# Kernel optimization log

Hardware: AMD Instinct MI355X
Metric: run time of the kernel (lower is better)

The kernel has to match this reference:

```python
import jax, jax.numpy as jnp
import numpy as np

B, S, D, H = 8, 384, 768, 12
MAX_POS = 512
P = 2 * MAX_POS - 1  # 1023


def setup_inputs() -> dict:
    key = jax.random.key(0)
    ks = jax.random.split(key, 14)
    w = 0.02
    return {
        "x": jax.random.normal(ks[0], (B, S, D), jnp.float32),
        "rel_pos_emb": jax.random.normal(ks[1], (P, D), jnp.float32),
        "Wq": jax.random.normal(ks[2], (D, D), jnp.float32) * w,
        "bq": jax.random.normal(ks[3], (D,), jnp.float32) * w,
        "Wk": jax.random.normal(ks[4], (D, D), jnp.float32) * w,
        "bk": jax.random.normal(ks[5], (D,), jnp.float32) * w,
        "Wv": jax.random.normal(ks[6], (D, D), jnp.float32) * w,
        "bv": jax.random.normal(ks[7], (D,), jnp.float32) * w,
        "q_bias": jax.random.normal(ks[8], (D,), jnp.float32) * w,
        "v_bias": jax.random.normal(ks[9], (D,), jnp.float32) * w,
        "Wpk": jax.random.normal(ks[10], (D, D), jnp.float32) * w,
        "Wpq": jax.random.normal(ks[11], (D, D), jnp.float32) * w,
        "Wo": jax.random.normal(ks[12], (D, D), jnp.float32) * w,
        "bo": jax.random.normal(ks[13], (D,), jnp.float32) * w,
    }


def reference(x, rel_pos_emb, Wq, bq, Wk, bk, Wv, bv, q_bias, v_bias, Wpk, Wpq, Wo, bo):
    b, s, d = x.shape
    dh = d // H
    scale = dh ** -0.5
    # relative position index: rel[i, j] = j - i + MAX_POS - 1
    rel = (jnp.arange(s)[None, :] - jnp.arange(s)[:, None]) + MAX_POS - 1
    emb = rel_pos_emb[rel]                      # [S, S, D]
    q = (x @ Wq + bq + q_bias).reshape(b, s, H, dh)
    k = (x @ Wk + bk).reshape(b, s, H, dh)
    v = (x @ Wv + bv + v_bias).reshape(b, s, H, dh)
    Kp = (emb @ Wpk).reshape(s, s, H, dh)       # pos keys   [i, j, h, d]
    Qp = (emb @ Wpq).reshape(s, s, H, dh)       # pos queries[i, j, h, d]
    c2c = jnp.einsum('bihd,bjhd->bhij', q, k)
    c2p = jnp.einsum('bihd,ijhd->bhij', q, Kp)
    p2c = jnp.einsum('ijhd,bjhd->bhij', Qp, k)
    scores = (c2c + c2p + p2c) * scale          # [B, H, S, S]
    w = jax.nn.softmax(scores, axis=-1)
    out = jnp.einsum('bhij,bjhd->bihd', w, v).reshape(b, s, d)
    return out @ Wo + bo
```

## Files before the change

kernel.cpp:

```cpp
#include <hip/hip_runtime.h>
#include <hip/hip_bf16.h>
#include <math.h>

#define BATCH 8
#define SEQ 384
#define DIM 768
#define NH 12
#define DH 64
#define NPOS 767
#define POS_OFF 128
#define NTOK (BATCH * SEQ)
#define QKN 1536
#define QKVN 2304
#define PN 1536

typedef __attribute__((ext_vector_type(8))) short short8;
typedef __attribute__((ext_vector_type(4))) float floatx4;
typedef unsigned int u32;

__device__ __forceinline__ ushort f2bf(float f) {
    __hip_bfloat16 h = __float2bfloat16(f);
    return *reinterpret_cast<ushort*>(&h);
}

__device__ __forceinline__ void gld16(const ushort* g, ushort* l) {
    __builtin_amdgcn_global_load_lds(
        (const __attribute__((address_space(1))) u32*)g,
        (__attribute__((address_space(3))) u32*)l, 16, 0, 0);
}

__global__ void cvt_all(const float* __restrict__ x, const float* __restrict__ rpe,
                        ushort* __restrict__ xb, ushort* __restrict__ rpeb) {
    int idx = blockIdx.x * 256 + threadIdx.x;
    const int n4x = NTOK * DIM / 4;
    const int n4p = NPOS * DIM / 4;
    const float* src; ushort* dst; int j;
    if (idx < n4x) { src = x; dst = xb; j = idx; }
    else if (idx < n4x + n4p) { src = rpe + (size_t)POS_OFF * DIM; dst = rpeb; j = idx - n4x; }
    else return;
    float4 f = ((const float4*)src)[j];
    ushort o[4] = {f2bf(f.x), f2bf(f.y), f2bf(f.z), f2bf(f.w)};
    *(uint2*)&dst[(size_t)j * 4] = *(uint2*)o;
}

__global__ __launch_bounds__(256) void cvt_transpose6(
    const float* W0, const float* W1, const float* W2,
    const float* W3, const float* W4, const float* W5,
    ushort* __restrict__ dst)
{
    __shared__ float t[64][65];
    const float* srcs[6] = {W0, W1, W2, W3, W4, W5};
    const float* in = srcs[blockIdx.z];
    ushort* out = dst + (size_t)blockIdx.z * DIM * DIM;
    const int tid = threadIdx.x;
    const int r0 = blockIdx.y * 64, c0 = blockIdx.x * 64;
    for (int p = 0; p < 16; ++p) {
        int e = tid + p * 256, i = e >> 6, j = e & 63;
        t[i][j] = in[(size_t)(r0 + i) * DIM + c0 + j];
    }
    __syncthreads();
    for (int p = 0; p < 16; ++p) {
        int e = tid + p * 256, i = e >> 6, j = e & 63;
        out[(size_t)(c0 + i) * DIM + r0 + j] = f2bf(t[j][i]);
    }
}

__global__ __launch_bounds__(256) void gemm128_qkv(
    const ushort* __restrict__ A, const ushort* __restrict__ Bt,
    const float* __restrict__ bq, const float* __restrict__ qbias,
    const float* __restrict__ bk, const float* __restrict__ bv,
    const float* __restrict__ vbias,
    ushort* __restrict__ qk, ushort* __restrict__ vT)
{
    __shared__ ushort As[128 * 64];
    __shared__ ushort Bs[128 * 64];
    const int tid = threadIdx.x;
    const int lane = tid & 63, w = tid >> 6;
    const int n0 = blockIdx.x * 128, m0 = blockIdx.y * 128;
    const int lr = lane >> 3;
    const int lc = (lane & 7) ^ (lr & 7);
    const ushort* ga[4]; const ushort* gb[4];
#pragma unroll
    for (int p = 0; p < 4; ++p) {
        int row = (w * 4 + p) * 8 + lr;
        ga[p] = A + (size_t)(m0 + row) * DIM + lc * 8;
        gb[p] = Bt + (size_t)(n0 + row) * DIM + lc * 8;
    }
    floatx4 acc[4][4] = {};
    const int qr = (w >> 1) * 64, qc = (w & 1) * 64;
    const int lm = lane & 15, lk = lane >> 4;
    for (int k0 = 0; k0 < DIM; k0 += 64) {
#pragma unroll
        for (int p = 0; p < 4; ++p) {
            gld16(ga[p], As + (w * 4 + p) * 512);
            gld16(gb[p], Bs + (w * 4 + p) * 512);
            ga[p] += 64; gb[p] += 64;
        }
        __syncthreads();
#pragma unroll
        for (int kk = 0; kk < 2; ++kk) {
            int ch = (kk * 4 + lk) ^ (lm & 7);
            short8 af[4], bf[4];
#pragma unroll
            for (int t = 0; t < 4; ++t) {
                af[t] = *(const short8*)&As[(qr + t * 16 + lm) * 64 + ch * 8];
                bf[t] = *(const short8*)&Bs[(qc + t * 16 + lm) * 64 + ch * 8];
            }
#pragma unroll
            for (int i = 0; i < 4; ++i)
#pragma unroll
                for (int j = 0; j < 4; ++j)
                    acc[i][j] = __builtin_amdgcn_mfma_f32_16x16x32_bf16(af[i], bf[j], acc[i][j], 0, 0, 0);
        }
        __syncthreads();
    }
#pragma unroll
    for (int i = 0; i < 4; ++i) {
        int mbase = m0 + qr + i * 16 + (lane >> 4) * 4;
        int bb = mbase / SEQ;
        int s0 = mbase - bb * SEQ;
#pragma unroll
        for (int j = 0; j < 4; ++j) {
            int n = n0 + qc + j * 16 + lm;
            float bs;
            if (n < 768) bs = bq[n] + qbias[n];
            else if (n < QKN) bs = bk[n - 768];
            else bs = bv[n - QKN] + vbias[n - QKN];
            if (n < QKN) {
#pragma unroll
                for (int r = 0; r < 4; ++r)
                    qk[(size_t)(mbase + r) * QKN + n] = f2bf(acc[i][j][r] + bs);
            } else {
                int c = n - QKN, h = c >> 6, d = c & 63;
                ushort tmp[4];
#pragma unroll
                for (int r = 0; r < 4; ++r) tmp[r] = f2bf(acc[i][j][r] + bs);
                *(uint2*)&vT[(((size_t)bb * NH + h) * DH + d) * SEQ + s0] = *(uint2*)tmp;
            }
        }
    }
}

__global__ __launch_bounds__(256) void gemm_bf16(
    const ushort* __restrict__ A, const ushort* __restrict__ Bt,
    const float* __restrict__ b1,
    float* __restrict__ outF, ushort* __restrict__ outB,
    int M, int N, int K)
{
    __shared__ ushort As[64][72];
    __shared__ ushort Bs[64][72];
    const int tid = threadIdx.x;
    const int lane = tid & 63, wave = tid >> 6;
    const int m0 = blockIdx.y * 64, n0 = blockIdx.x * 64;
    floatx4 acc[4] = {};
    for (int k0 = 0; k0 < K; k0 += 64) {
        for (int p = 0; p < 2; ++p) {
            int e = tid + p * 256;
            int m = e >> 3, k8 = e & 7;
            uint4 val = {0, 0, 0, 0};
            if (m0 + m < M) val = *(const uint4*)(A + (size_t)(m0 + m) * K + k0 + k8 * 8);
            *(uint4*)&As[m][k8 * 8] = val;
            *(uint4*)&Bs[m][k8 * 8] = *(const uint4*)(Bt + (size_t)(n0 + m) * K + k0 + k8 * 8);
        }
        __syncthreads();
#pragma unroll
        for (int kk = 0; kk < 64; kk += 32) {
            short8 a = *(const short8*)&As[wave * 16 + (lane & 15)][kk + (lane >> 4) * 8];
#pragma unroll
            for (int c = 0; c < 4; ++c) {
                short8 b = *(const short8*)&Bs[c * 16 + (lane & 15)][kk + (lane >> 4) * 8];
                acc[c] = __builtin_amdgcn_mfma_f32_16x16x32_bf16(a, b, acc[c], 0, 0, 0);
            }
        }
        __syncthreads();
    }
#pragma unroll
    for (int c = 0; c < 4; ++c) {
        int col = n0 + c * 16 + (lane & 15);
        float bias = b1 ? b1[col] : 0.f;
#pragma unroll
        for (int r = 0; r < 4; ++r) {
            int row = m0 + wave * 16 + (lane >> 4) * 4 + r;
            if (row >= M) continue;
            float v = acc[c][r] + bias;
            if (outF) outF[(size_t)row * N + col] = v;
            if (outB) outB[(size_t)row * N + col] = f2bf(v);
        }
    }
}

__global__ __launch_bounds__(512, 4) void attn_fused2(
    const ushort* __restrict__ qk, const ushort* __restrict__ vT,
    const ushort* __restrict__ posKQ, ushort* __restrict__ aob)
{
    __shared__ ushort qs[64 * 64];
    __shared__ ushort kt[64 * 64];
    __shared__ ushort kps[128 * 64];
    __shared__ ushort qps[128 * 64];
    __shared__ ushort vtt[64 * 64];
    __shared__ alignas(16) char smem_st[64 * 66 * 4];
    __shared__ float rowsum[64];
    float* st = (float*)smem_st;
    ushort* pt = (ushort*)smem_st;

    const int tid = threadIdx.x;
    const int lane = tid & 63, w = tid >> 6;
    const int i0 = blockIdx.x * 64;
    const int h = blockIdx.y, b = blockIdx.z;
    const int lm = lane & 15, lq = lane >> 4;
    const int lr = lane >> 3, l8 = lane & 7;
    const int lc = l8 ^ (lr & 7);

    if (tid < 64) rowsum[tid] = 0.f;

    gld16(qk + (size_t)(b * SEQ + i0 + 8 * w + lr) * QKN + h * DH + lc * 8, qs + w * 512);
    const ushort* kb = qk + 768 + h * DH;
    const ushort* vb = vT + ((size_t)b * NH + h) * DH * SEQ;

    floatx4 occ[2] = {};
    const int exr = tid >> 3, exseg = tid & 7;

    for (int jt = 0; jt < 6; ++jt) {
        const int j0 = jt * 64;
        const int t0 = j0 - i0 + 320;
        gld16(kb + (size_t)(b * SEQ + j0 + 8 * w + lr) * QKN + lc * 8, kt + w * 512);
        gld16(posKQ + (size_t)(t0 + 16 * w + lr) * PN + h * DH + lc * 8, kps + w * 1024);
        gld16(posKQ + (size_t)(t0 + 16 * w + 8 + lr) * PN + h * DH + lc * 8, kps + w * 1024 + 512);
        gld16(posKQ + (size_t)(t0 + 16 * w + lr) * PN + 768 + h * DH + lc * 8, qps + w * 1024);
        gld16(posKQ + (size_t)(t0 + 16 * w + 8 + lr) * PN + 768 + h * DH + lc * 8, qps + w * 1024 + 512);
        gld16(vb + (size_t)(8 * w + lr) * SEQ + j0 + lc * 8, vtt + w * 512);
        __syncthreads();

#pragma unroll
        for (int s = 0; s < 2; ++s) {
            int idx = w * 2 + s, tr = idx >> 2, tc = idx & 3;
            floatx4 a = {};
#pragma unroll
            for (int kk = 0; kk < 2; ++kk) {
                int ch = (kk * 4 + lq) ^ (lm & 7);
                short8 av = *(const short8*)&qs[(tr * 16 + lm) * 64 + ch * 8];
                short8 bv = *(const short8*)&kt[(tc * 16 + lm) * 64 + ch * 8];
                a = __builtin_amdgcn_mfma_f32_16x16x32_bf16(av, bv, a, 0, 0, 0);
            }
            int col = tc * 16 + lm;
#pragma unroll
            for (int r = 0; r < 4; ++r)
                st[(tr * 16 + lq * 4 + r) * 66 + col] = a[r];
        }
        __syncthreads();

#pragma unroll
        for (int s = 0; s < 4; ++s) {
            int idx = w * 4 + s, tr = idx >> 3, tc = idx & 7;
            floatx4 a = {};
#pragma unroll
            for (int kk = 0; kk < 2; ++kk) {
                int ch = (kk * 4 + lq) ^ (lm & 7);
                short8 av = *(const short8*)&qs[(tr * 16 + lm) * 64 + ch * 8];
                short8 bv = *(const short8*)&kps[(tc * 16 + lm) * 64 + ch * 8];
                a = __builtin_amdgcn_mfma_f32_16x16x32_bf16(av, bv, a, 0, 0, 0);
            }
            int t = tc * 16 + lm;
#pragma unroll
            for (int r = 0; r < 4; ++r) {
                int il = tr * 16 + lq * 4 + r;
                int jl = t + il - 63;
                if ((unsigned)jl < 64u) st[il * 66 + jl] += a[r];
            }
        }
        __syncthreads();

#pragma unroll
        for (int s = 0; s < 4; ++s) {
            int idx = w * 4 + s, tr = idx >> 2, tc = idx & 3;
            floatx4 a = {};
#pragma unroll
            for (int kk = 0; kk < 2; ++kk) {
                int ch = (kk * 4 + lq) ^ (lm & 7);
                short8 av = *(const short8*)&qps[(tr * 16 + lm) * 64 + ch * 8];
                short8 bv = *(const short8*)&kt[(tc * 16 + lm) * 64 + ch * 8];
                a = __builtin_amdgcn_mfma_f32_16x16x32_bf16(av, bv, a, 0, 0, 0);
            }
            int jl = tc * 16 + lm;
#pragma unroll
            for (int r = 0; r < 4; ++r) {
                int t = tr * 16 + lq * 4 + r;
                int il = jl - t + 63;
                if ((unsigned)il < 64u) st[il * 66 + jl] += a[r];
            }
        }
        __syncthreads();

        float p[8];
        {
            float psum = 0.f;
#pragma unroll
            for (int c = 0; c < 8; ++c) {
                float sv = st[exr * 66 + exseg * 8 + c] * 0.125f;
                p[c] = __expf(sv);
                psum += p[c];
            }
            psum += __shfl_xor(psum, 1);
            psum += __shfl_xor(psum, 2);
            psum += __shfl_xor(psum, 4);
            if (exseg == 0) rowsum[exr] += psum;
        }
        __syncthreads();
        {
            ushort tmp[8];
#pragma unroll
            for (int c = 0; c < 8; ++c) tmp[c] = f2bf(p[c]);
            int ch = exseg ^ (exr & 7);
            *(uint4*)&pt[exr * 64 + ch * 8] = *(uint4*)tmp;
        }
        __syncthreads();

#pragma unroll
        for (int s = 0; s < 2; ++s) {
            int idx = w * 2 + s, tr = idx >> 2, tc = idx & 3;
#pragma unroll
            for (int kk = 0; kk < 2; ++kk) {
                int ch = (kk * 4 + lq) ^ (lm & 7);
                short8 av = *(const short8*)&pt[(tr * 16 + lm) * 64 + ch * 8];
                short8 bv = *(const short8*)&vtt[(tc * 16 + lm) * 64 + ch * 8];
                occ[s] = __builtin_amdgcn_mfma_f32_16x16x32_bf16(av, bv, occ[s], 0, 0, 0);
            }
        }
        __syncthreads();
    }

#pragma unroll
    for (int s = 0; s < 2; ++s) {
        int idx = w * 2 + s, tr = idx >> 2, tc = idx & 3;
#pragma unroll
        for (int r = 0; r < 4; ++r) {
            int row = tr * 16 + lq * 4 + r;
            float ov = occ[s][r] / rowsum[row];
            aob[(size_t)(b * SEQ + i0 + row) * DIM + h * DH + tc * 16 + lm] = f2bf(ov);
        }
    }
}

extern "C" void kernel_launch(void* const* d_in, const int* in_sizes, int n_in,
                              void* d_out, int out_size, void* d_ws, size_t ws_size,
                              hipStream_t stream) {
    const float* x   = (const float*)d_in[0];
    const float* rpe = (const float*)d_in[1];
    const float* Wq  = (const float*)d_in[2];
    const float* bq  = (const float*)d_in[3];
    const float* Wk  = (const float*)d_in[4];
    const float* bk  = (const float*)d_in[5];
    const float* Wv  = (const float*)d_in[6];
    const float* bv  = (const float*)d_in[7];
    const float* qbias = (const float*)d_in[8];
    const float* vbias = (const float*)d_in[9];
    const float* Wpk = (const float*)d_in[10];
    const float* Wpq = (const float*)d_in[11];
    const float* Wo  = (const float*)d_in[12];
    const float* bo  = (const float*)d_in[13];
    float* out = (float*)d_out;

    char* ws = (char*)d_ws;
    ushort* xb    = (ushort*)ws; ws += (size_t)NTOK * DIM * 2;
    ushort* qkbuf = (ushort*)ws; ws += (size_t)NTOK * QKN * 2;
    ushort* vT    = (ushort*)ws; ws += (size_t)NTOK * DIM * 2;
    ushort* aob   = (ushort*)ws; ws += (size_t)NTOK * DIM * 2;
    ushort* rpeb  = (ushort*)ws; ws += (size_t)NPOS * DIM * 2;
    ushort* posKQ = (ushort*)ws; ws += (size_t)NPOS * PN * 2;
    ushort* wsT   = (ushort*)ws; ws += (size_t)6 * DIM * DIM * 2;

    dim3 b256(256);
    {
        int n4 = NTOK * DIM / 4 + NPOS * DIM / 4;
        cvt_all<<<(n4 + 255) / 256, b256, 0, stream>>>(x, rpe, xb, rpeb);
        cvt_transpose6<<<dim3(DIM / 64, DIM / 64, 6), b256, 0, stream>>>(Wq, Wk, Wv, Wpk, Wpq, Wo, wsT);
    }
    gemm128_qkv<<<dim3(QKVN / 128, NTOK / 128), b256, 0, stream>>>(
        xb, wsT, bq, qbias, bk, bv, vbias, qkbuf, vT);
    gemm_bf16<<<dim3(PN / 64, (NPOS + 63) / 64), b256, 0, stream>>>(
        rpeb, wsT + (size_t)3 * DIM * DIM, nullptr, nullptr, posKQ, NPOS, PN, DIM);
    attn_fused2<<<dim3(SEQ / 64, NH, BATCH), dim3(512), 0, stream>>>(qkbuf, vT, posKQ, aob);
    gemm_bf16<<<dim3(DIM / 64, NTOK / 64), b256, 0, stream>>>(
        aob, wsT + (size_t)5 * DIM * DIM, bo, out, nullptr, NTOK, DIM, DIM);
}
```

Baseline: 207.3 us.

## Use 128x128 GEMM tiles and merge attention score passes via LDS atomics

Replaces the 64x64 generic GEMM with a 128x128 tile version that uses swizzled direct global-to-LDS loads and a 4x4 MFMA accumulator per wave, used for both the position projection and the output projection. In attention, the three score contributions (c2c, c2p, p2c) are now accumulated into a zeroed LDS score tile with atomicAdd, which removes the barriers between the passes. The softmax exp and bf16 store are merged into one phase, and P is written into the kps buffer. This trades fewer barriers and more reuse per tile against LDS atomic overhead, fewer GEMM blocks (lower occupancy on the small GEMMs), and an extra zeroing pass each iteration.

New measurement: 476.6 us. +129.9%, slower.

```diff
diff --git a/kernel.cpp b/kernel.cpp
--- a/kernel.cpp
+++ b/kernel.cpp
@@ -141,55 +141,75 @@
     }
 }
 
-__global__ __launch_bounds__(256) void gemm_bf16(
+__global__ __launch_bounds__(256) void gemm128(
     const ushort* __restrict__ A, const ushort* __restrict__ Bt,
-    const float* __restrict__ b1,
+    const float* __restrict__ bias,
     float* __restrict__ outF, ushort* __restrict__ outB,
     int M, int N, int K)
 {
-    __shared__ ushort As[64][72];
-    __shared__ ushort Bs[64][72];
+    __shared__ ushort As[128 * 64];
+    __shared__ ushort Bs[128 * 64];
     const int tid = threadIdx.x;
-    const int lane = tid & 63, wave = tid >> 6;
-    const int m0 = blockIdx.y * 64, n0 = blockIdx.x * 64;
-    floatx4 acc[4] = {};
+    const int lane = tid & 63, w = tid >> 6;
+    const int n0 = blockIdx.x * 128, m0 = blockIdx.y * 128;
+    const int lr = lane >> 3;
+    const int lc = (lane & 7) ^ (lr & 7);
+    const ushort* ga[4]; const ushort* gb[4];
+#pragma unroll
+    for (int p = 0; p < 4; ++p) {
+        int row = (w * 4 + p) * 8 + lr;
+        int arow = m0 + row; if (arow > M - 1) arow = M - 1;
+        ga[p] = A + (size_t)arow * K + lc * 8;
+        gb[p] = Bt + (size_t)(n0 + row) * K + lc * 8;
+    }
+    floatx4 acc[4][4] = {};
+    const int qr = (w >> 1) * 64, qc = (w & 1) * 64;
+    const int lm = lane & 15, lk = lane >> 4;
     for (int k0 = 0; k0 < K; k0 += 64) {
-        for (int p = 0; p < 2; ++p) {
-            int e = tid + p * 256;
-            int m = e >> 3, k8 = e & 7;
-            uint4 val = {0, 0, 0, 0};
-            if (m0 + m < M) val = *(const uint4*)(A + (size_t)(m0 + m) * K + k0 + k8 * 8);
-            *(uint4*)&As[m][k8 * 8] = val;
-            *(uint4*)&Bs[m][k8 * 8] = *(const uint4*)(Bt + (size_t)(n0 + m) * K + k0 + k8 * 8);
-        }
-        __syncthreads();
-#pragma unroll
-        for (int kk = 0; kk < 64; kk += 32) {
-            short8 a = *(const short8*)&As[wave * 16 + (lane & 15)][kk + (lane >> 4) * 8];
-#pragma unroll
-            for (int c = 0; c < 4; ++c) {
-                short8 b = *(const short8*)&Bs[c * 16 + (lane & 15)][kk + (lane >> 4) * 8];
-                acc[c] = __builtin_amdgcn_mfma_f32_16x16x32_bf16(a, b, acc[c], 0, 0, 0);
-            }
-        }
-        __syncthreads();
-    }
-#pragma unroll
-    for (int c = 0; c < 4; ++c) {
-        int col = n0 + c * 16 + (lane & 15);
-        float bias = b1 ? b1[col] : 0.f;
-#pragma unroll
-        for (int r = 0; r < 4; ++r) {
-            int row = m0 + wave * 16 + (lane >> 4) * 4 + r;
-            if (row >= M) continue;
-            float v = acc[c][r] + bias;
-            if (outF) outF[(size_t)row * N + col] = v;
-            if (outB) outB[(size_t)row * N + col] = f2bf(v);
-        }
-    }
-}
-
-__global__ __launch_bounds__(512, 4) void attn_fused2(
+#pragma unroll
+        for (int p = 0; p < 4; ++p) {
+            gld16(ga[p], As + (w * 4 + p) * 512);
+            gld16(gb[p], Bs + (w * 4 + p) * 512);
+            ga[p] += 64; gb[p] += 64;
+        }
+        __syncthreads();
+#pragma unroll
+        for (int kk = 0; kk < 2; ++kk) {
+            int ch = (kk * 4 + lk) ^ (lm & 7);
+            short8 af[4], bf[4];
+#pragma unroll
+            for (int t = 0; t < 4; ++t) {
+                af[t] = *(const short8*)&As[(qr + t * 16 + lm) * 64 + ch * 8];
+                bf[t] = *(const short8*)&Bs[(qc + t * 16 + lm) * 64 + ch * 8];
+            }
+#pragma unroll
+            for (int i = 0; i < 4; ++i)
+#pragma unroll
+                for (int j = 0; j < 4; ++j)
+                    acc[i][j] = __builtin_amdgcn_mfma_f32_16x16x32_bf16(af[i], bf[j], acc[i][j], 0, 0, 0);
+        }
+        __syncthreads();
+    }
+#pragma unroll
+    for (int i = 0; i < 4; ++i) {
+        int mbase = m0 + qr + i * 16 + (lane >> 4) * 4;
+#pragma unroll
+        for (int j = 0; j < 4; ++j) {
+            int n = n0 + qc + j * 16 + lm;
+            float bs = bias ? bias[n] : 0.f;
+#pragma unroll
+            for (int r = 0; r < 4; ++r) {
+                int row = mbase + r;
+                if (row >= M) continue;
+                float v = acc[i][j][r] + bs;
+                if (outF) outF[(size_t)row * N + n] = v;
+                else outB[(size_t)row * N + n] = f2bf(v);
+            }
+        }
+    }
+}
+
+__global__ __launch_bounds__(512, 4) void attn_fused3(
     const ushort* __restrict__ qk, const ushort* __restrict__ vT,
     const ushort* __restrict__ posKQ, ushort* __restrict__ aob)
 {
@@ -198,10 +218,9 @@
     __shared__ ushort kps[128 * 64];
     __shared__ ushort qps[128 * 64];
     __shared__ ushort vtt[64 * 64];
-    __shared__ alignas(16) char smem_st[64 * 66 * 4];
+    __shared__ float st[64 * 68];
     __shared__ float rowsum[64];
-    float* st = (float*)smem_st;
-    ushort* pt = (ushort*)smem_st;
+    ushort* pt = kps;
 
     const int tid = threadIdx.x;
     const int lane = tid & 63, w = tid >> 6;
@@ -229,6 +248,8 @@
         gld16(posKQ + (size_t)(t0 + 16 * w + lr) * PN + 768 + h * DH + lc * 8, qps + w * 1024);
         gld16(posKQ + (size_t)(t0 + 16 * w + 8 + lr) * PN + 768 + h * DH + lc * 8, qps + w * 1024 + 512);
         gld16(vb + (size_t)(8 * w + lr) * SEQ + j0 + lc * 8, vtt + w * 512);
+        for (int z = tid; z < 64 * 68 / 4; z += 512)
+            *(float4*)&st[z * 4] = float4{0.f, 0.f, 0.f, 0.f};
         __syncthreads();
 
 #pragma unroll
@@ -245,10 +266,8 @@
             int col = tc * 16 + lm;
 #pragma unroll
             for (int r = 0; r < 4; ++r)
-                st[(tr * 16 + lq * 4 + r) * 66 + col] = a[r];
-        }
-        __syncthreads();
-
+                atomicAdd(&st[(tr * 16 + lq * 4 + r) * 68 + col], a[r]);
+        }
 #pragma unroll
         for (int s = 0; s < 4; ++s) {
             int idx = w * 4 + s, tr = idx >> 3, tc = idx & 7;
@@ -265,11 +284,9 @@
             for (int r = 0; r < 4; ++r) {
                 int il = tr * 16 + lq * 4 + r;
                 int jl = t + il - 63;
-                if ((unsigned)jl < 64u) st[il * 66 + jl] += a[r];
-            }
-        }
-        __syncthreads();
-
+                if ((unsigned)jl < 64u) atomicAdd(&st[il * 68 + jl], a[r]);
+            }
+        }
 #pragma unroll
         for (int s = 0; s < 4; ++s) {
             int idx = w * 4 + s, tr = idx >> 2, tc = idx & 3;
@@ -286,27 +303,24 @@
             for (int r = 0; r < 4; ++r) {
                 int t = tr * 16 + lq * 4 + r;
                 int il = jl - t + 63;
-                if ((unsigned)il < 64u) st[il * 66 + jl] += a[r];
-            }
-        }
-        __syncthreads();
-
-        float p[8];
+                if ((unsigned)il < 64u) atomicAdd(&st[il * 68 + jl], a[r]);
+            }
+        }
+        __syncthreads();
+
         {
-            float psum = 0.f;
-#pragma unroll
-            for (int c = 0; c < 8; ++c) {
-                float sv = st[exr * 66 + exseg * 8 + c] * 0.125f;
-                p[c] = __expf(sv);
-                psum += p[c];
-            }
+            float4 sv0 = *(const float4*)&st[exr * 68 + exseg * 8];
+            float4 sv1 = *(const float4*)&st[exr * 68 + exseg * 8 + 4];
+            float p[8];
+            p[0] = __expf(sv0.x * 0.125f); p[1] = __expf(sv0.y * 0.125f);
+            p[2] = __expf(sv0.z * 0.125f); p[3] = __expf(sv0.w * 0.125f);
+            p[4] = __expf(sv1.x * 0.125f); p[5] = __expf(sv1.y * 0.125f);
+            p[6] = __expf(sv1.z * 0.125f); p[7] = __expf(sv1.w * 0.125f);
+            float psum = p[0] + p[1] + p[2] + p[3] + p[4] + p[5] + p[6] + p[7];
             psum += __shfl_xor(psum, 1);
             psum += __shfl_xor(psum, 2);
             psum += __shfl_xor(psum, 4);
             if (exseg == 0) rowsum[exr] += psum;
-        }
-        __syncthreads();
-        {
             ushort tmp[8];
 #pragma unroll
             for (int c = 0; c < 8; ++c) tmp[c] = f2bf(p[c]);
@@ -377,9 +391,9 @@
     }
     gemm128_qkv<<<dim3(QKVN / 128, NTOK / 128), b256, 0, stream>>>(
         xb, wsT, bq, qbias, bk, bv, vbias, qkbuf, vT);
-    gemm_bf16<<<dim3(PN / 64, (NPOS + 63) / 64), b256, 0, stream>>>(
+    gemm128<<<dim3(PN / 128, (NPOS + 127) / 128), b256, 0, stream>>>(
         rpeb, wsT + (size_t)3 * DIM * DIM, nullptr, nullptr, posKQ, NPOS, PN, DIM);
-    attn_fused2<<<dim3(SEQ / 64, NH, BATCH), dim3(512), 0, stream>>>(qkbuf, vT, posKQ, aob);
-    gemm_bf16<<<dim3(DIM / 64, NTOK / 64), b256, 0, stream>>>(
+    attn_fused3<<<dim3(SEQ / 64, NH, BATCH), dim3(512), 0, stream>>>(qkbuf, vT, posKQ, aob);
+    gemm128<<<dim3(DIM / 128, NTOK / 128), b256, 0, stream>>>(
         aob, wsT + (size_t)5 * DIM * DIM, bo, out, nullptr, NTOK, DIM, DIM);
 }
```
